# Kernel optimization log

Measured on AMD Instinct MI355X. Metric: run time of the kernel, lower is better.

## Reference

```python
import jax, jax.numpy as jnp
import numpy as np
import math

H = 16          # attn_heads
DK = 64         # features_dec // attn_heads
NEG = -1e9      # additive causal mask value
EPS = 1e-6      # LayerNorm eps (annotated transformer)


def get_slopes(n):
    def p2(m):
        start = 2.0 ** (-(2.0 ** (-(math.log2(m) - 3))))
        return [start * start ** i for i in range(m)]
    if math.log2(n).is_integer():
        return p2(n)
    cp = 2 ** math.floor(math.log2(n))
    return p2(cp) + get_slopes(2 * cp)[0::2][: n - cp]


def setup_inputs() -> dict:
    key = jax.random.key(0)
    ks = jax.random.split(key, 12)
    B, S, FT, FDZ, FDEC, FD = 8, 1024, 16, 768, 1024, 16

    def lin(k, out_d, in_d):
        return jax.random.normal(k, (out_d, in_d), jnp.float32) / np.float32(np.sqrt(in_d))

    return {
        "z_sample": jax.random.normal(ks[0], (B, FDZ), jnp.float32),
        "r_traj": jax.random.normal(ks[1], (B, S, FT), jnp.float32),
        "dense_w": lin(ks[2], FDEC, FDZ + FT), "dense_b": jnp.zeros((FDEC,), jnp.float32),
        "ln_g": jnp.ones((FDEC,), jnp.float32), "ln_b": jnp.zeros((FDEC,), jnp.float32),
        "wq": lin(ks[3], FDEC, FDEC), "bq": jnp.zeros((FDEC,), jnp.float32),
        "wk": lin(ks[4], FDEC, FDEC), "bk": jnp.zeros((FDEC,), jnp.float32),
        "wv": lin(ks[5], FDEC, FDEC), "bv": jnp.zeros((FDEC,), jnp.float32),
        "wo": lin(ks[6], FDEC, FDEC), "bo": jnp.zeros((FDEC,), jnp.float32),
        "dec_w": lin(ks[7], FD, FDEC), "dec_b": jnp.zeros((FD,), jnp.float32),
    }


def reference(z_sample, r_traj, dense_w, dense_b, ln_g, ln_b,
              wq, bq, wk, bk, wv, bv, wo, bo, dec_w, dec_b):
    B, S, _ = r_traj.shape
    # concat trajectory features with broadcast latent sample -> [B,S,in_size]
    x = jnp.concatenate(
        [r_traj, jnp.broadcast_to(z_sample[:, None, :], (B, S, z_sample.shape[-1]))], axis=-1)
    x = x @ dense_w.T + dense_b  # [B,S,FDEC]

    # causal additive mask + ALiBi bias: bias[h,i,j] = causal(i,j) + slope_h * j
    slopes = jnp.asarray(get_slopes(H), jnp.float32)
    causal = jnp.triu(jnp.full((S, S), NEG, jnp.float32), k=1)
    bias = causal[None, :, :] + slopes[:, None, None] * jnp.arange(S, dtype=jnp.float32)[None, None, :]  # [H,S,S]

    # pre-norm sublayer: x + attn(LN(x))  (dropout=0 / eval)
    mu = x.mean(-1, keepdims=True)
    var = x.var(-1, keepdims=True)
    xn = ln_g * (x - mu) / jnp.sqrt(var + EPS) + ln_b

    def heads(w, b):
        return (xn @ w.T + b).reshape(B, S, H, DK).transpose(0, 2, 1, 3)  # [B,H,S,DK]

    q, k, v = heads(wq, bq), heads(wk, bk), heads(wv, bv)
    scores = jnp.einsum('bhid,bhjd->bhij', q, k) / np.float32(np.sqrt(DK)) + bias[None]
    attn = jax.nn.softmax(scores, axis=-1)
    o = jnp.einsum('bhij,bhjd->bhid', attn, v).transpose(0, 2, 1, 3).reshape(B, S, H * DK)
    x = x + o @ wo.T + bo

    # decode_state then transpose(-2,-1) -> [B, features_d, S]
    return (x @ dec_w.T + dec_b).transpose(0, 2, 1)
```

## Files before the change

kernel.cpp:

```cpp
#include <hip/hip_runtime.h>

static constexpr int Bn   = 8;
static constexpr int S    = 1024;
static constexpr int FT   = 16;
static constexpr int FDZ  = 768;
static constexpr int INK  = 784;
static constexpr int FDEC = 1024;
static constexpr int M    = Bn * S;
static constexpr int H    = 16;
static constexpr int FD   = 16;

typedef __bf16 bf16x8 __attribute__((ext_vector_type(8)));
typedef float  f32x4  __attribute__((ext_vector_type(4)));

__device__ __forceinline__ unsigned short f2b(float f) {
  return __builtin_bit_cast(unsigned short, static_cast<__bf16>(f));
}
__device__ __forceinline__ float b2f(unsigned short u) {
  return (float)__builtin_bit_cast(__bf16, u);
}

__device__ __forceinline__ void gload16(const void* g, void* l) {
  __builtin_amdgcn_global_load_lds(
      (const __attribute__((address_space(1))) unsigned int*)g,
      (__attribute__((address_space(3))) unsigned int*)l, 16, 0, 0);
}

__global__ __launch_bounds__(256) void k_prep(const float* __restrict__ dnw,
                                              const float* __restrict__ wq,
                                              const float* __restrict__ wk,
                                              const float* __restrict__ wv,
                                              const float* __restrict__ wo,
                                              const float* __restrict__ dcw,
                                              const float* __restrict__ bq,
                                              const float* __restrict__ bk,
                                              const float* __restrict__ bv,
                                              unsigned short* __restrict__ w3,
                                              unsigned short* __restrict__ wob,
                                              unsigned short* __restrict__ dwb,
                                              float* __restrict__ b3,
                                              unsigned short* __restrict__ wt16) {
  const int bid = blockIdx.x, tid = threadIdx.x;
  const int c = tid * 4;
  if (bid < 3072) {
    const int r = bid;
    const float* src = (r < 1024) ? wq : (r < 2048 ? wk : wv);
    const int rr = r & 1023;
    float4 v = *reinterpret_cast<const float4*>(&src[(size_t)rr * 1024 + c]);
    unsigned short o4[4] = {f2b(v.x), f2b(v.y), f2b(v.z), f2b(v.w)};
    *reinterpret_cast<uint2*>(&w3[(size_t)r * 1024 + c]) = *reinterpret_cast<uint2*>(o4);
  } else if (bid < 4096) {
    const int r = bid - 3072;
    float4 v = *reinterpret_cast<const float4*>(&wo[(size_t)r * 1024 + c]);
    unsigned short o4[4] = {f2b(v.x), f2b(v.y), f2b(v.z), f2b(v.w)};
    *reinterpret_cast<uint2*>(&wob[(size_t)r * 1024 + c]) = *reinterpret_cast<uint2*>(o4);
  } else if (bid < 4112) {
    const int r = bid - 4096;
    float4 v = *reinterpret_cast<const float4*>(&dcw[(size_t)r * 1024 + c]);
    unsigned short o4[4] = {f2b(v.x), f2b(v.y), f2b(v.z), f2b(v.w)};
    *reinterpret_cast<uint2*>(&dwb[(size_t)r * 1024 + c]) = *reinterpret_cast<uint2*>(o4);
  } else if (bid < 4115) {
    const int r = bid - 4112;
    const float* s = (r == 0) ? bq : (r == 1 ? bk : bv);
    *reinterpret_cast<float4*>(&b3[r * 1024 + c]) =
        *reinterpret_cast<const float4*>(&s[c]);
  } else {
    const int idx = (bid - 4115) * 256 + tid;
    const int k = idx >> 10, cc = idx & 1023;
    wt16[k * 1024 + cc] = f2b(dnw[(size_t)cc * INK + k]);
  }
}

__global__ __launch_bounds__(256) void k_za(const float* __restrict__ z,
                                            const float* __restrict__ dnw,
                                            float* __restrict__ za) {
  const int tid = threadIdx.x, lane = tid & 63, w = tid >> 6;
  const int idx = blockIdx.x * 4 + w;
  const int col = idx >> 3, b = idx & 7;
  const float* wp = &dnw[(size_t)col * INK + FT];
  const float* zp = &z[b * FDZ];
  float s = 0.f;
#pragma unroll
  for (int i = 0; i < 12; i++) {
    int k = lane + i * 64;
    s += wp[k] * zp[k];
  }
  for (int off = 32; off; off >>= 1) s += __shfl_down(s, off);
  if (lane == 0) za[b * 1024 + col] = s;
}

__global__ __launch_bounds__(256) void k_dense_ln(const float* __restrict__ rt,
                                                  const float* __restrict__ za,
                                                  const float* __restrict__ dnb,
                                                  const float* __restrict__ lng,
                                                  const float* __restrict__ lnb,
                                                  const unsigned short* __restrict__ wt16g,
                                                  unsigned short* __restrict__ xres,
                                                  unsigned short* __restrict__ xn) {
  __shared__ unsigned short wt[16 * 1024];
  __shared__ float ss[4], qq[4];
  const int tid = threadIdx.x, lane = tid & 63, wv = tid >> 6;
  const int c0 = tid * 4;
#pragma unroll
  for (int i = 0; i < 8; i++)
    reinterpret_cast<uint4*>(wt)[tid + 256 * i] =
        reinterpret_cast<const uint4*>(wt16g)[tid + 256 * i];
  const float4 bv  = *reinterpret_cast<const float4*>(&dnb[c0]);
  const float4 gv  = *reinterpret_cast<const float4*>(&lng[c0]);
  const float4 bev = *reinterpret_cast<const float4*>(&lnb[c0]);
  __syncthreads();

  for (int r = 0; r < 4; ++r) {
    const int m = blockIdx.x * 4 + r;
    const int b = m >> 10;
    float rtv[16];
    {
      float4 t0 = *reinterpret_cast<const float4*>(&rt[m * 16 + 0]);
      float4 t1 = *reinterpret_cast<const float4*>(&rt[m * 16 + 4]);
      float4 t2 = *reinterpret_cast<const float4*>(&rt[m * 16 + 8]);
      float4 t3 = *reinterpret_cast<const float4*>(&rt[m * 16 + 12]);
      rtv[0]=t0.x; rtv[1]=t0.y; rtv[2]=t0.z; rtv[3]=t0.w;
      rtv[4]=t1.x; rtv[5]=t1.y; rtv[6]=t1.z; rtv[7]=t1.w;
      rtv[8]=t2.x; rtv[9]=t2.y; rtv[10]=t2.z; rtv[11]=t2.w;
      rtv[12]=t3.x; rtv[13]=t3.y; rtv[14]=t3.z; rtv[15]=t3.w;
    }
    float4 zav = *reinterpret_cast<const float4*>(&za[b * 1024 + c0]);
    float acc[4] = {zav.x + bv.x, zav.y + bv.y, zav.z + bv.z, zav.w + bv.w};
#pragma unroll
    for (int k = 0; k < 16; ++k) {
      uint2 wraw = *reinterpret_cast<const uint2*>(&wt[k * 1024 + c0]);
      const unsigned short* wp = reinterpret_cast<const unsigned short*>(&wraw);
      float rk = rtv[k];
      acc[0] += rk * b2f(wp[0]);
      acc[1] += rk * b2f(wp[1]);
      acc[2] += rk * b2f(wp[2]);
      acc[3] += rk * b2f(wp[3]);
    }
    float s = acc[0] + acc[1] + acc[2] + acc[3];
    float q = acc[0]*acc[0] + acc[1]*acc[1] + acc[2]*acc[2] + acc[3]*acc[3];
    for (int off = 32; off; off >>= 1) { s += __shfl_down(s, off); q += __shfl_down(q, off); }
    if (lane == 0) { ss[wv] = s; qq[wv] = q; }
    __syncthreads();
    float St = ss[0] + ss[1] + ss[2] + ss[3];
    float Qt = qq[0] + qq[1] + qq[2] + qq[3];
    float mu  = St * (1.f / 1024.f);
    float var = Qt * (1.f / 1024.f) - mu * mu;
    float rstd = rsqrtf(var + 1e-6f);
    unsigned short xo[4], no[4];
    xo[0] = f2b(acc[0]); no[0] = f2b(gv.x * (acc[0] - mu) * rstd + bev.x);
    xo[1] = f2b(acc[1]); no[1] = f2b(gv.y * (acc[1] - mu) * rstd + bev.y);
    xo[2] = f2b(acc[2]); no[2] = f2b(gv.z * (acc[2] - mu) * rstd + bev.z);
    xo[3] = f2b(acc[3]); no[3] = f2b(gv.w * (acc[3] - mu) * rstd + bev.w);
    *reinterpret_cast<uint2*>(&xres[(size_t)m * 1024 + c0]) = *reinterpret_cast<uint2*>(xo);
    *reinterpret_cast<uint2*>(&xn[(size_t)m * 1024 + c0])   = *reinterpret_cast<uint2*>(no);
    __syncthreads();
  }
}

template<int EPI>
__global__ __launch_bounds__(512, 4) void k_gemm2(const unsigned short* __restrict__ A, int lda,
                                                  const unsigned short* __restrict__ Bw, int ldb,
                                                  int K, int N,
                                                  const float* __restrict__ bias,
                                                  float* __restrict__ Cf,
                                                  unsigned short* __restrict__ Cb) {
  __shared__ __align__(16) unsigned short As[3 * 256 * 32];
  __shared__ __align__(16) unsigned short Bs[3 * 128 * 32];
  const int tid = threadIdx.x, lane = tid & 63, w = tid >> 6;
  const int wr = w >> 1, wc = w & 1;
  const int lr = lane & 15, lg = lane >> 4;

  const int xcd = blockIdx.x & 7;
  const int j   = blockIdx.x >> 3;
  const int m0  = (xcd * 4 + (j & 3)) * 256;
  const int n0  = (j >> 2) * 128;

  const int nt = K >> 5;

  const int giA0 = w * 64 + lane;
  const int rA0 = giA0 >> 2, cA0 = (giA0 & 3) ^ ((rA0 >> 1) & 3);
  const int giA1 = 512 + w * 64 + lane;
  const int rA1 = giA1 >> 2, cA1 = (giA1 & 3) ^ ((rA1 >> 1) & 3);
  const int giB0 = w * 64 + lane;
  const int rB0 = giB0 >> 2, cB0 = (giB0 & 3) ^ ((rB0 >> 1) & 3);
  const unsigned short* srcA0 = A + (size_t)(m0 + rA0) * lda + cA0 * 8;
  const unsigned short* srcA1 = A + (size_t)(m0 + rA1) * lda + cA1 * 8;
  const unsigned short* srcB0 = Bw + (size_t)(n0 + rB0) * ldb + cB0 * 8;
  const int dA0 = (w * 64) * 8;
  const int dA1 = (512 + w * 64) * 8;
  const int dB0 = (w * 64) * 8;

  int offA[4], offB[4];
#pragma unroll
  for (int mi = 0; mi < 4; mi++) {
    int r = wr * 64 + mi * 16 + lr;
    offA[mi] = r * 32 + (lg ^ ((r >> 1) & 3)) * 8;
  }
#pragma unroll
  for (int ni = 0; ni < 4; ni++) {
    int r = wc * 64 + ni * 16 + lr;
    offB[ni] = r * 32 + (lg ^ ((r >> 1) & 3)) * 8;
  }

  f32x4 acc[4][4];
#pragma unroll
  for (int i = 0; i < 4; i++)
#pragma unroll
    for (int j2 = 0; j2 < 4; j2++)
#pragma unroll
      for (int e = 0; e < 4; e++) acc[i][j2][e] = 0.f;

  auto stage = [&](int tt) {
    const int sl = tt % 3;
    const size_t ko = (size_t)tt * 32;
    gload16(srcA0 + ko, &As[sl * 8192 + dA0]);
    gload16(srcA1 + ko, &As[sl * 8192 + dA1]);
    gload16(srcB0 + ko, &Bs[sl * 4096 + dB0]);
  };
  auto compute = [&](int tt) {
    const int sa = (tt % 3) * 8192;
    const int sb = (tt % 3) * 4096;
    bf16x8 af[4], bfr[4];
#pragma unroll
    for (int mi = 0; mi < 4; mi++)
      af[mi] = *reinterpret_cast<const bf16x8*>(&As[sa + offA[mi]]);
#pragma unroll
    for (int ni = 0; ni < 4; ni++)
      bfr[ni] = *reinterpret_cast<const bf16x8*>(&Bs[sb + offB[ni]]);
    __builtin_amdgcn_s_setprio(1);
#pragma unroll
    for (int mi = 0; mi < 4; mi++)
#pragma unroll
      for (int ni = 0; ni < 4; ni++)
        acc[mi][ni] = __builtin_amdgcn_mfma_f32_16x16x32_bf16(af[mi], bfr[ni], acc[mi][ni], 0, 0, 0);
    __builtin_amdgcn_s_setprio(0);
  };

  stage(0); stage(1);

  int t = 0;
  for (; t < nt - 2; ++t) {
    asm volatile("s_waitcnt vmcnt(3)" ::: "memory");
    __builtin_amdgcn_s_barrier();
    stage(t + 2);
    compute(t);
  }
  asm volatile("s_waitcnt vmcnt(3)" ::: "memory");
  __builtin_amdgcn_s_barrier();
  compute(t); ++t;
  asm volatile("s_waitcnt vmcnt(0)" ::: "memory");
  __builtin_amdgcn_s_barrier();
  compute(t);

#pragma unroll
  for (int mi = 0; mi < 4; mi++)
#pragma unroll
    for (int ni = 0; ni < 4; ni++) {
      int col = n0 + wc * 64 + ni * 16 + lr;
      float bv = bias ? bias[col] : 0.f;
#pragma unroll
      for (int jj = 0; jj < 4; jj++) {
        int row = m0 + wr * 64 + mi * 16 + lg * 4 + jj;
        float v = acc[mi][ni][jj] + bv;
        if constexpr (EPI == 0) {
          Cf[(size_t)row * N + col] = v;
        } else {
          Cb[(size_t)row * N + col] = f2b(v);
        }
      }
    }
}

template<int EPI>
__global__ __launch_bounds__(256, 3) void k_gemm1(const unsigned short* __restrict__ A, int lda,
                                                  const unsigned short* __restrict__ Bw, int ldb,
                                                  int K, int N,
                                                  const float* __restrict__ bias,
                                                  const unsigned short* __restrict__ res,
                                                  unsigned short* __restrict__ Cb) {
  __shared__ __align__(16) unsigned short As[3 * 128 * 32];
  __shared__ __align__(16) unsigned short Bs[3 * 128 * 32];
  const int tid = threadIdx.x, lane = tid & 63, w = tid >> 6;
  const int wr = w >> 1, wc = w & 1;
  const int lr = lane & 15, lg = lane >> 4;

  const int xcd = blockIdx.x & 7;
  const int j   = blockIdx.x >> 3;
  const int m0  = (xcd * 8 + (j & 7)) * 128;
  const int n0  = (j >> 3) * 128;

  const int nt = K >> 5;

  const int g0 = tid;
  const int r0g = g0 >> 2, c0g = (g0 & 3) ^ ((r0g >> 1) & 3);
  const int g1 = tid + 256;
  const int r1g = g1 >> 2, c1g = (g1 & 3) ^ ((r1g >> 1) & 3);
  const unsigned short* srcA0 = A + (size_t)(m0 + r0g) * lda + c0g * 8;
  const unsigned short* srcA1 = A + (size_t)(m0 + r1g) * lda + c1g * 8;
  const unsigned short* srcB0 = Bw + (size_t)(n0 + r0g) * ldb + c0g * 8;
  const unsigned short* srcB1 = Bw + (size_t)(n0 + r1g) * ldb + c1g * 8;
  const int d0 = (w * 64) * 8;
  const int d1 = (256 + w * 64) * 8;

  int offA[4], offB[4];
#pragma unroll
  for (int mi = 0; mi < 4; mi++) {
    int r = wr * 64 + mi * 16 + lr;
    offA[mi] = r * 32 + (lg ^ ((r >> 1) & 3)) * 8;
  }
#pragma unroll
  for (int ni = 0; ni < 4; ni++) {
    int r = wc * 64 + ni * 16 + lr;
    offB[ni] = r * 32 + (lg ^ ((r >> 1) & 3)) * 8;
  }

  f32x4 acc[4][4];
#pragma unroll
  for (int i = 0; i < 4; i++)
#pragma unroll
    for (int j2 = 0; j2 < 4; j2++)
#pragma unroll
      for (int e = 0; e < 4; e++) acc[i][j2][e] = 0.f;

  auto stage = [&](int tt) {
    const int sl = tt % 3;
    const size_t ko = (size_t)tt * 32;
    gload16(srcA0 + ko, &As[sl * 4096 + d0]);
    gload16(srcA1 + ko, &As[sl * 4096 + d1]);
    gload16(srcB0 + ko, &Bs[sl * 4096 + d0]);
    gload16(srcB1 + ko, &Bs[sl * 4096 + d1]);
  };
  auto compute = [&](int tt) {
    const int sl = (tt % 3) * 4096;
    bf16x8 af[4], bfr[4];
#pragma unroll
    for (int mi = 0; mi < 4; mi++)
      af[mi] = *reinterpret_cast<const bf16x8*>(&As[sl + offA[mi]]);
#pragma unroll
    for (int ni = 0; ni < 4; ni++)
      bfr[ni] = *reinterpret_cast<const bf16x8*>(&Bs[sl + offB[ni]]);
    __builtin_amdgcn_s_setprio(1);
#pragma unroll
    for (int mi = 0; mi < 4; mi++)
#pragma unroll
      for (int ni = 0; ni < 4; ni++)
        acc[mi][ni] = __builtin_amdgcn_mfma_f32_16x16x32_bf16(af[mi], bfr[ni], acc[mi][ni], 0, 0, 0);
    __builtin_amdgcn_s_setprio(0);
  };

  stage(0); stage(1);

  int t = 0;
  for (; t < nt - 2; ++t) {
    asm volatile("s_waitcnt vmcnt(4)" ::: "memory");
    __builtin_amdgcn_s_barrier();
    stage(t + 2);
    compute(t);
  }
  asm volatile("s_waitcnt vmcnt(4)" ::: "memory");
  __builtin_amdgcn_s_barrier();
  compute(t); ++t;
  asm volatile("s_waitcnt vmcnt(0)" ::: "memory");
  __builtin_amdgcn_s_barrier();
  compute(t);

#pragma unroll
  for (int mi = 0; mi < 4; mi++)
#pragma unroll
    for (int ni = 0; ni < 4; ni++) {
      int col = n0 + wc * 64 + ni * 16 + lr;
      float bv = bias ? bias[col] : 0.f;
#pragma unroll
      for (int jj = 0; jj < 4; jj++) {
        int row = m0 + wr * 64 + mi * 16 + lg * 4 + jj;
        float v = acc[mi][ni][jj] + bv;
        size_t o = (size_t)row * N + col;
        if constexpr (EPI == 2) {
          Cb[o] = f2b(b2f(res[o]) + v);
        } else {
          Cb[o] = f2b(v);
        }
      }
    }
}

__global__ __launch_bounds__(512, 4) void k_attn(const unsigned short* __restrict__ qkv,
                                                 unsigned short* __restrict__ o) {
  __shared__ unsigned short Ks[2][64][72];
  __shared__ unsigned short Vt[2][64][72];
  __shared__ unsigned short Pl[8][16][72];
  const int tid = threadIdx.x, lane = tid & 63, w = tid >> 6;
  const int bh = blockIdx.x, b = bh >> 4, h = bh & 15;
  const int lr = lane & 15, lg = lane >> 4, lg4 = lg * 4;
  const int krow = tid >> 3, c8 = (tid & 7) << 3;
  const int kb8 = krow >> 3, kl = krow & 7, vq = tid & 7;
  const float slope2 = exp2f(-0.5f * (float)(h + 1)) * 1.44269504f;
  const float sc2 = 0.125f * 1.44269504f;

  for (int ph = 0; ph < 2; ++ph) {
    const int qb = ph ? (7 - (int)blockIdx.y) : (int)blockIdx.y;
    const int q0 = qb * 128;
    const int qlo = q0 + w * 16;
    const int qa = qlo + lr;

    bf16x8 qf0, qf1;
    {
      const unsigned short* qp = &qkv[(size_t)(b * 1024 + qlo + lr) * 3072 + h * 64];
      qf0 = *reinterpret_cast<const bf16x8*>(qp + lg * 8);
      qf1 = *reinterpret_cast<const bf16x8*>(qp + 32 + lg * 8);
    }
    float mrun = -3.0e38f, lrun = 0.f;
    f32x4 accO[4];
    for (int dn = 0; dn < 4; dn++)
      for (int e = 0; e < 4; e++) accO[dn][e] = 0.f;

    const int nt = 2 * qb + 2;
    uint4 kr, vr;
    {
      const size_t base = (size_t)(b * 1024 + krow) * 3072 + h * 64;
      kr = *reinterpret_cast<const uint4*>(&qkv[base + 1024 + c8]);
      vr = *reinterpret_cast<const uint4*>(&qkv[base + 2048 + c8]);
    }
    *reinterpret_cast<uint4*>(&Ks[0][krow][c8]) = kr;
    {
      const unsigned short* vs = reinterpret_cast<const unsigned short*>(&vr);
      for (int jj = 0; jj < 8; jj++)
        Vt[0][c8 + jj][((kb8 ^ vq) << 3) | kl] = vs[jj];
    }
    __syncthreads();

    for (int kt = 0; kt < nt; ++kt) {
      const int kb = kt << 6;
      const int cb = kt & 1, nb = cb ^ 1;
      const bool hn = (kt + 1 < nt);
      if (hn) {
        const size_t base = (size_t)(b * 1024 + kb + 64 + krow) * 3072 + h * 64;
        kr = *reinterpret_cast<const uint4*>(&qkv[base + 1024 + c8]);
        vr = *reinterpret_cast<const uint4*>(&qkv[base + 2048 + c8]);
      }
      const bool act = (kb <= qlo + 15);
      float f = 1.f;
      if (act) {
        f32x4 sf[4];
        for (int kn = 0; kn < 4; kn++) {
          f32x4 zz;
          for (int e = 0; e < 4; e++) zz[e] = 0.f;
          bf16x8 kf0 = *reinterpret_cast<const bf16x8*>(&Ks[cb][kn * 16 + lr][lg * 8]);
          bf16x8 kf1 = *reinterpret_cast<const bf16x8*>(&Ks[cb][kn * 16 + lr][32 + lg * 8]);
          zz = __builtin_amdgcn_mfma_f32_16x16x32_bf16(kf0, qf0, zz, 0, 0, 0);
          zz = __builtin_amdgcn_mfma_f32_16x16x32_bf16(kf1, qf1, zz, 0, 0, 0);
          sf[kn] = zz;
        }
        const bool needmask = (kb + 63 > qlo);
        float sc[4][4];
        float ml = -3.0e38f;
        for (int kn = 0; kn < 4; kn++) {
          float alib = slope2 * (float)(kb + kn * 16 + lg4);
          for (int jj = 0; jj < 4; jj++) {
            float v = fmaf(sf[kn][jj], sc2, alib + slope2 * (float)jj);
            if (needmask && (kb + kn * 16 + lg4 + jj > qa)) v = -3.0e38f;
            sc[kn][jj] = v;
            ml = fmaxf(ml, v);
          }
        }
        ml = fmaxf(ml, __shfl_xor(ml, 16));
        ml = fmaxf(ml, __shfl_xor(ml, 32));
        float mnew = fmaxf(mrun, ml);
        f = exp2f(mrun - mnew);
        float rs = 0.f;
        for (int kn = 0; kn < 4; kn++) {
          __bf16 pb[4];
          for (int jj = 0; jj < 4; jj++) {
            float pv = exp2f(sc[kn][jj] - mnew);
            rs += pv;
            pb[jj] = (__bf16)pv;
          }
          *reinterpret_cast<uint2*>(&Pl[w][lr][kn * 16 + lg4]) =
              *reinterpret_cast<uint2*>(pb);
        }
        rs += __shfl_xor(rs, 16);
        rs += __shfl_xor(rs, 32);
        lrun = lrun * f + rs;
        mrun = mnew;
      }
      if (hn) {
        *reinterpret_cast<uint4*>(&Ks[nb][krow][c8]) = kr;
        const unsigned short* vs = reinterpret_cast<const unsigned short*>(&vr);
        for (int jj = 0; jj < 8; jj++)
          Vt[nb][c8 + jj][((kb8 ^ vq) << 3) | kl] = vs[jj];
      }
      if (act) {
        float fj[4];
        for (int jj = 0; jj < 4; jj++) fj[jj] = __shfl(f, (lane & 48) | (lg4 + jj));
        for (int dn = 0; dn < 4; dn++)
          for (int jj = 0; jj < 4; jj++) accO[dn][jj] *= fj[jj];
        asm volatile("s_waitcnt lgkmcnt(0)" ::: "memory");
        for (int ks = 0; ks < 2; ks++) {
          bf16x8 pa = *reinterpret_cast<const bf16x8*>(&Pl[w][lr][ks * 32 + lg * 8]);
          for (int dn = 0; dn < 4; dn++) {
            int d = dn * 16 + lr;
            bf16x8 vb = *reinterpret_cast<const bf16x8*>(
                &Vt[cb][d][(((ks * 4 + lg) ^ (d >> 3)) << 3)]);
            accO[dn] = __builtin_amdgcn_mfma_f32_16x16x32_bf16(pa, vb, accO[dn], 0, 0, 0);
          }
        }
      }
      __syncthreads();
    }
    float linv[4];
    for (int jj = 0; jj < 4; jj++)
      linv[jj] = 1.f / __shfl(lrun, (lane & 48) | (lg4 + jj));
    for (int dn = 0; dn < 4; dn++)
      for (int jj = 0; jj < 4; jj++) {
        int row = qlo + lg4 + jj;
        int d = dn * 16 + lr;
        o[(size_t)(b * 1024 + row) * 1024 + h * 64 + d] = f2b(accO[dn][jj] * linv[jj]);
      }
  }
}

__global__ __launch_bounds__(256) void k_dec(const unsigned short* __restrict__ xb,
                                             const unsigned short* __restrict__ dw,
                                             const float* __restrict__ db,
                                             float* __restrict__ out) {
  const int tid = threadIdx.x, lane = tid & 63, w = tid >> 6;
  const int lr = lane & 15, lg = lane >> 4;
  const int sb = blockIdx.x * 4 + w;
  const int r0 = sb * 16;
  f32x4 acc;
  for (int e = 0; e < 4; e++) acc[e] = 0.f;
  const unsigned short* arow = &xb[(size_t)(r0 + lr) * 1024];
  const unsigned short* brow = &dw[(size_t)lr * 1024];
  for (int k0 = 0; k0 < 1024; k0 += 32) {
    bf16x8 af = *reinterpret_cast<const bf16x8*>(arow + k0 + lg * 8);
    bf16x8 bf = *reinterpret_cast<const bf16x8*>(brow + k0 + lg * 8);
    acc = __builtin_amdgcn_mfma_f32_16x16x32_bf16(af, bf, acc, 0, 0, 0);
  }
  const int b = r0 >> 10;
  const int sl = (r0 & 1023) + lg * 4;
  float bias = db[lr];
  float4 res;
  res.x = acc[0] + bias; res.y = acc[1] + bias; res.z = acc[2] + bias; res.w = acc[3] + bias;
  *reinterpret_cast<float4*>(&out[(size_t)(b * 16 + lr) * 1024 + sl]) = res;
}

extern "C" void kernel_launch(void* const* d_in, const int* in_sizes, int n_in,
                              void* d_out, int out_size, void* d_ws, size_t ws_size,
                              hipStream_t stream) {
  (void)in_sizes; (void)n_in; (void)out_size;
  const float* z   = (const float*)d_in[0];
  const float* rt  = (const float*)d_in[1];
  const float* dnw = (const float*)d_in[2];
  const float* dnb = (const float*)d_in[3];
  const float* lng = (const float*)d_in[4];
  const float* lnb = (const float*)d_in[5];
  const float* wq  = (const float*)d_in[6];
  const float* bq  = (const float*)d_in[7];
  const float* wk  = (const float*)d_in[8];
  const float* bk  = (const float*)d_in[9];
  const float* wv  = (const float*)d_in[10];
  const float* bv  = (const float*)d_in[11];
  const float* wo  = (const float*)d_in[12];
  const float* bo  = (const float*)d_in[13];
  const float* dcw = (const float*)d_in[14];
  const float* dcb = (const float*)d_in[15];
  float* out = (float*)d_out;

  char* p = (char*)d_ws;
  unsigned short* xres = (unsigned short*)p; p += (size_t)M * FDEC * 2;
  unsigned short* xn   = (unsigned short*)p; p += (size_t)M * FDEC * 2;
  unsigned short* w3   = (unsigned short*)p; p += (size_t)3 * FDEC * FDEC * 2;
  float* b3            = (float*)p;          p += (size_t)3 * FDEC * 4;
  unsigned short* qkv  = (unsigned short*)p; p += (size_t)M * 3 * FDEC * 2;
  unsigned short* ob   = (unsigned short*)p; p += (size_t)M * FDEC * 2;
  unsigned short* wob  = (unsigned short*)p; p += (size_t)FDEC * FDEC * 2;
  unsigned short* dwb  = (unsigned short*)p; p += (size_t)FD * FDEC * 2;
  float* za            = (float*)p;          p += (size_t)8 * 1024 * 4;
  unsigned short* wt16 = (unsigned short*)p; p += (size_t)16 * 1024 * 2;
  if ((size_t)(p - (char*)d_ws) > ws_size) return;

  k_prep<<<4179, 256, 0, stream>>>(dnw, wq, wk, wv, wo, dcw, bq, bk, bv,
                                   w3, wob, dwb, b3, wt16);
  k_za<<<2048, 256, 0, stream>>>(z, dnw, za);
  k_dense_ln<<<2048, 256, 0, stream>>>(rt, za, dnb, lng, lnb, wt16, xres, xn);
  k_gemm2<1><<<(M / 256) * (3 * FDEC / 128), 512, 0, stream>>>(xn, FDEC, w3, FDEC, FDEC, 3 * FDEC, b3, nullptr, qkv);
  k_attn<<<dim3(Bn * H, 4), 512, 0, stream>>>(qkv, ob);
  k_gemm1<2><<<(M / 128) * (FDEC / 128), 256, 0, stream>>>(ob, FDEC, wob, FDEC, FDEC, FDEC, bo, xres, xn);
  k_dec<<<M / 64, 256, 0, stream>>>(xn, dwb, dcb, out);
}
```

Baseline: 185.5 us.

## Fold output projection into decoder via precombined weight, drop O-projection GEMM

Because the decoder is linear, dec_w·(x + o·Woᵀ + bo) is rewritten as dec_w·x + (dec_w·Wo)·o + (dec_w·bo + dec_b). A new kernel builds the 16x1024 combined weight and bias, so the full 8192x1024x1024 output-projection GEMM goes away and the decoder kernel does two thin K=1024 MFMA passes instead. The QKV projection also switches from the 256x128-tile gemm2 kernel to the 128x128-tile gemm1 kernel. In exchange, the combined weight is rounded to bf16 and a strided weight reduction runs on every call.

```diff
diff --git a/kernel.cpp b/kernel.cpp
--- a/kernel.cpp
+++ b/kernel.cpp
@@ -30,13 +30,11 @@
                                               const float* __restrict__ wq,
                                               const float* __restrict__ wk,
                                               const float* __restrict__ wv,
-                                              const float* __restrict__ wo,
                                               const float* __restrict__ dcw,
                                               const float* __restrict__ bq,
                                               const float* __restrict__ bk,
                                               const float* __restrict__ bv,
                                               unsigned short* __restrict__ w3,
-                                              unsigned short* __restrict__ wob,
                                               unsigned short* __restrict__ dwb,
                                               float* __restrict__ b3,
                                               unsigned short* __restrict__ wt16) {
@@ -49,25 +47,55 @@
     float4 v = *reinterpret_cast<const float4*>(&src[(size_t)rr * 1024 + c]);
     unsigned short o4[4] = {f2b(v.x), f2b(v.y), f2b(v.z), f2b(v.w)};
     *reinterpret_cast<uint2*>(&w3[(size_t)r * 1024 + c]) = *reinterpret_cast<uint2*>(o4);
-  } else if (bid < 4096) {
+  } else if (bid < 3088) {
     const int r = bid - 3072;
-    float4 v = *reinterpret_cast<const float4*>(&wo[(size_t)r * 1024 + c]);
-    unsigned short o4[4] = {f2b(v.x), f2b(v.y), f2b(v.z), f2b(v.w)};
-    *reinterpret_cast<uint2*>(&wob[(size_t)r * 1024 + c]) = *reinterpret_cast<uint2*>(o4);
-  } else if (bid < 4112) {
-    const int r = bid - 4096;
     float4 v = *reinterpret_cast<const float4*>(&dcw[(size_t)r * 1024 + c]);
     unsigned short o4[4] = {f2b(v.x), f2b(v.y), f2b(v.z), f2b(v.w)};
     *reinterpret_cast<uint2*>(&dwb[(size_t)r * 1024 + c]) = *reinterpret_cast<uint2*>(o4);
-  } else if (bid < 4115) {
-    const int r = bid - 4112;
+  } else if (bid < 3091) {
+    const int r = bid - 3088;
     const float* s = (r == 0) ? bq : (r == 1 ? bk : bv);
     *reinterpret_cast<float4*>(&b3[r * 1024 + c]) =
         *reinterpret_cast<const float4*>(&s[c]);
   } else {
-    const int idx = (bid - 4115) * 256 + tid;
+    const int idx = (bid - 3091) * 256 + tid;
     const int k = idx >> 10, cc = idx & 1023;
     wt16[k * 1024 + cc] = f2b(dnw[(size_t)cc * INK + k]);
+  }
+}
+
+__global__ __launch_bounds__(256) void k_wcomb(const float* __restrict__ dcw,
+                                               const float* __restrict__ wo,
+                                               const float* __restrict__ bo,
+                                               const float* __restrict__ dcb,
+                                               unsigned short* __restrict__ wcombb,
+                                               float* __restrict__ bias2) {
+  const int tid = threadIdx.x, lane = tid & 63, w = tid >> 6;
+  if (blockIdx.x < 4096) {
+    const int idx = blockIdx.x * 4 + w;
+    const int i = idx >> 10, jcol = idx & 1023;
+    const float* dp = &dcw[(size_t)i * 1024];
+    float s = 0.f;
+#pragma unroll
+    for (int t = 0; t < 16; t++) {
+      int k = lane + t * 64;
+      s += dp[k] * wo[(size_t)k * 1024 + jcol];
+    }
+    for (int off = 32; off; off >>= 1) s += __shfl_down(s, off);
+    if (lane == 0) wcombb[i * 1024 + jcol] = f2b(s);
+  } else {
+    for (int q = 0; q < 4; q++) {
+      int f = w * 4 + q;
+      const float* dp = &dcw[(size_t)f * 1024];
+      float s = 0.f;
+#pragma unroll
+      for (int t = 0; t < 16; t++) {
+        int k = lane + t * 64;
+        s += dp[k] * bo[k];
+      }
+      for (int off = 32; off; off >>= 1) s += __shfl_down(s, off);
+      if (lane == 0) bias2[f] = s + dcb[f];
+    }
   }
 }
 
@@ -158,125 +186,10 @@
 }
 
 template<int EPI>
-__global__ __launch_bounds__(512, 4) void k_gemm2(const unsigned short* __restrict__ A, int lda,
-                                                  const unsigned short* __restrict__ Bw, int ldb,
-                                                  int K, int N,
-                                                  const float* __restrict__ bias,
-                                                  float* __restrict__ Cf,
-                                                  unsigned short* __restrict__ Cb) {
-  __shared__ __align__(16) unsigned short As[3 * 256 * 32];
-  __shared__ __align__(16) unsigned short Bs[3 * 128 * 32];
-  const int tid = threadIdx.x, lane = tid & 63, w = tid >> 6;
-  const int wr = w >> 1, wc = w & 1;
-  const int lr = lane & 15, lg = lane >> 4;
-
-  const int xcd = blockIdx.x & 7;
-  const int j   = blockIdx.x >> 3;
-  const int m0  = (xcd * 4 + (j & 3)) * 256;
-  const int n0  = (j >> 2) * 128;
-
-  const int nt = K >> 5;
-
-  const int giA0 = w * 64 + lane;
-  const int rA0 = giA0 >> 2, cA0 = (giA0 & 3) ^ ((rA0 >> 1) & 3);
-  const int giA1 = 512 + w * 64 + lane;
-  const int rA1 = giA1 >> 2, cA1 = (giA1 & 3) ^ ((rA1 >> 1) & 3);
-  const int giB0 = w * 64 + lane;
-  const int rB0 = giB0 >> 2, cB0 = (giB0 & 3) ^ ((rB0 >> 1) & 3);
-  const unsigned short* srcA0 = A + (size_t)(m0 + rA0) * lda + cA0 * 8;
-  const unsigned short* srcA1 = A + (size_t)(m0 + rA1) * lda + cA1 * 8;
-  const unsigned short* srcB0 = Bw + (size_t)(n0 + rB0) * ldb + cB0 * 8;
-  const int dA0 = (w * 64) * 8;
-  const int dA1 = (512 + w * 64) * 8;
-  const int dB0 = (w * 64) * 8;
-
-  int offA[4], offB[4];
-#pragma unroll
-  for (int mi = 0; mi < 4; mi++) {
-    int r = wr * 64 + mi * 16 + lr;
-    offA[mi] = r * 32 + (lg ^ ((r >> 1) & 3)) * 8;
-  }
-#pragma unroll
-  for (int ni = 0; ni < 4; ni++) {
-    int r = wc * 64 + ni * 16 + lr;
-    offB[ni] = r * 32 + (lg ^ ((r >> 1) & 3)) * 8;
-  }
-
-  f32x4 acc[4][4];
-#pragma unroll
-  for (int i = 0; i < 4; i++)
-#pragma unroll
-    for (int j2 = 0; j2 < 4; j2++)
-#pragma unroll
-      for (int e = 0; e < 4; e++) acc[i][j2][e] = 0.f;
-
-  auto stage = [&](int tt) {
-    const int sl = tt % 3;
-    const size_t ko = (size_t)tt * 32;
-    gload16(srcA0 + ko, &As[sl * 8192 + dA0]);
-    gload16(srcA1 + ko, &As[sl * 8192 + dA1]);
-    gload16(srcB0 + ko, &Bs[sl * 4096 + dB0]);
-  };
-  auto compute = [&](int tt) {
-    const int sa = (tt % 3) * 8192;
-    const int sb = (tt % 3) * 4096;
-    bf16x8 af[4], bfr[4];
-#pragma unroll
-    for (int mi = 0; mi < 4; mi++)
-      af[mi] = *reinterpret_cast<const bf16x8*>(&As[sa + offA[mi]]);
-#pragma unroll
-    for (int ni = 0; ni < 4; ni++)
-      bfr[ni] = *reinterpret_cast<const bf16x8*>(&Bs[sb + offB[ni]]);
-    __builtin_amdgcn_s_setprio(1);
-#pragma unroll
-    for (int mi = 0; mi < 4; mi++)
-#pragma unroll
-      for (int ni = 0; ni < 4; ni++)
-        acc[mi][ni] = __builtin_amdgcn_mfma_f32_16x16x32_bf16(af[mi], bfr[ni], acc[mi][ni], 0, 0, 0);
-    __builtin_amdgcn_s_setprio(0);
-  };
-
-  stage(0); stage(1);
-
-  int t = 0;
-  for (; t < nt - 2; ++t) {
-    asm volatile("s_waitcnt vmcnt(3)" ::: "memory");
-    __builtin_amdgcn_s_barrier();
-    stage(t + 2);
-    compute(t);
-  }
-  asm volatile("s_waitcnt vmcnt(3)" ::: "memory");
-  __builtin_amdgcn_s_barrier();
-  compute(t); ++t;
-  asm volatile("s_waitcnt vmcnt(0)" ::: "memory");
-  __builtin_amdgcn_s_barrier();
-  compute(t);
-
-#pragma unroll
-  for (int mi = 0; mi < 4; mi++)
-#pragma unroll
-    for (int ni = 0; ni < 4; ni++) {
-      int col = n0 + wc * 64 + ni * 16 + lr;
-      float bv = bias ? bias[col] : 0.f;
-#pragma unroll
-      for (int jj = 0; jj < 4; jj++) {
-        int row = m0 + wr * 64 + mi * 16 + lg * 4 + jj;
-        float v = acc[mi][ni][jj] + bv;
-        if constexpr (EPI == 0) {
-          Cf[(size_t)row * N + col] = v;
-        } else {
-          Cb[(size_t)row * N + col] = f2b(v);
-        }
-      }
-    }
-}
-
-template<int EPI>
 __global__ __launch_bounds__(256, 3) void k_gemm1(const unsigned short* __restrict__ A, int lda,
                                                   const unsigned short* __restrict__ Bw, int ldb,
                                                   int K, int N,
                                                   const float* __restrict__ bias,
-                                                  const unsigned short* __restrict__ res,
                                                   unsigned short* __restrict__ Cb) {
   __shared__ __align__(16) unsigned short As[3 * 128 * 32];
   __shared__ __align__(16) unsigned short Bs[3 * 128 * 32];
@@ -374,12 +287,7 @@
       for (int jj = 0; jj < 4; jj++) {
         int row = m0 + wr * 64 + mi * 16 + lg * 4 + jj;
         float v = acc[mi][ni][jj] + bv;
-        size_t o = (size_t)row * N + col;
-        if constexpr (EPI == 2) {
-          Cb[o] = f2b(b2f(res[o]) + v);
-        } else {
-          Cb[o] = f2b(v);
-        }
+        Cb[(size_t)row * N + col] = f2b(v);
       }
     }
 }
@@ -519,26 +427,33 @@
   }
 }
 
-__global__ __launch_bounds__(256) void k_dec(const unsigned short* __restrict__ xb,
-                                             const unsigned short* __restrict__ dw,
-                                             const float* __restrict__ db,
-                                             float* __restrict__ out) {
+__global__ __launch_bounds__(256) void k_dec2(const unsigned short* __restrict__ xres,
+                                              const unsigned short* __restrict__ ob,
+                                              const unsigned short* __restrict__ dwb,
+                                              const unsigned short* __restrict__ wcombb,
+                                              const float* __restrict__ bias2,
+                                              float* __restrict__ out) {
   const int tid = threadIdx.x, lane = tid & 63, w = tid >> 6;
   const int lr = lane & 15, lg = lane >> 4;
   const int sb = blockIdx.x * 4 + w;
   const int r0 = sb * 16;
   f32x4 acc;
   for (int e = 0; e < 4; e++) acc[e] = 0.f;
-  const unsigned short* arow = &xb[(size_t)(r0 + lr) * 1024];
-  const unsigned short* brow = &dw[(size_t)lr * 1024];
+  const unsigned short* arow1 = &xres[(size_t)(r0 + lr) * 1024];
+  const unsigned short* arow2 = &ob[(size_t)(r0 + lr) * 1024];
+  const unsigned short* brow1 = &dwb[(size_t)lr * 1024];
+  const unsigned short* brow2 = &wcombb[(size_t)lr * 1024];
   for (int k0 = 0; k0 < 1024; k0 += 32) {
-    bf16x8 af = *reinterpret_cast<const bf16x8*>(arow + k0 + lg * 8);
-    bf16x8 bf = *reinterpret_cast<const bf16x8*>(brow + k0 + lg * 8);
-    acc = __builtin_amdgcn_mfma_f32_16x16x32_bf16(af, bf, acc, 0, 0, 0);
+    bf16x8 a1 = *reinterpret_cast<const bf16x8*>(arow1 + k0 + lg * 8);
+    bf16x8 b1 = *reinterpret_cast<const bf16x8*>(brow1 + k0 + lg * 8);
+    acc = __builtin_amdgcn_mfma_f32_16x16x32_bf16(a1, b1, acc, 0, 0, 0);
+    bf16x8 a2 = *reinterpret_cast<const bf16x8*>(arow2 + k0 + lg * 8);
+    bf16x8 b2 = *reinterpret_cast<const bf16x8*>(brow2 + k0 + lg * 8);
+    acc = __builtin_amdgcn_mfma_f32_16x16x32_bf16(a2, b2, acc, 0, 0, 0);
   }
   const int b = r0 >> 10;
   const int sl = (r0 & 1023) + lg * 4;
-  float bias = db[lr];
+  float bias = bias2[lr];
   float4 res;
   res.x = acc[0] + bias; res.y = acc[1] + bias; res.z = acc[2] + bias; res.w = acc[3] + bias;
   *reinterpret_cast<float4*>(&out[(size_t)(b * 16 + lr) * 1024 + sl]) = res;
@@ -567,24 +482,25 @@
   float* out = (float*)d_out;
 
   char* p = (char*)d_ws;
-  unsigned short* xres = (unsigned short*)p; p += (size_t)M * FDEC * 2;
-  unsigned short* xn   = (unsigned short*)p; p += (size_t)M * FDEC * 2;
-  unsigned short* w3   = (unsigned short*)p; p += (size_t)3 * FDEC * FDEC * 2;
-  float* b3            = (float*)p;          p += (size_t)3 * FDEC * 4;
-  unsigned short* qkv  = (unsigned short*)p; p += (size_t)M * 3 * FDEC * 2;
-  unsigned short* ob   = (unsigned short*)p; p += (size_t)M * FDEC * 2;
-  unsigned short* wob  = (unsigned short*)p; p += (size_t)FDEC * FDEC * 2;
-  unsigned short* dwb  = (unsigned short*)p; p += (size_t)FD * FDEC * 2;
-  float* za            = (float*)p;          p += (size_t)8 * 1024 * 4;
-  unsigned short* wt16 = (unsigned short*)p; p += (size_t)16 * 1024 * 2;
+  unsigned short* xres  = (unsigned short*)p; p += (size_t)M * FDEC * 2;
+  unsigned short* xn    = (unsigned short*)p; p += (size_t)M * FDEC * 2;
+  unsigned short* w3    = (unsigned short*)p; p += (size_t)3 * FDEC * FDEC * 2;
+  float* b3             = (float*)p;          p += (size_t)3 * FDEC * 4;
+  unsigned short* qkv   = (unsigned short*)p; p += (size_t)M * 3 * FDEC * 2;
+  unsigned short* ob    = (unsigned short*)p; p += (size_t)M * FDEC * 2;
+  unsigned short* dwb   = (unsigned short*)p; p += (size_t)FD * FDEC * 2;
+  unsigned short* wcombb= (unsigned short*)p; p += (size_t)FD * FDEC * 2;
+  float* bias2          = (float*)p;          p += (size_t)FD * 4;
+  float* za             = (float*)p;          p += (size_t)8 * 1024 * 4;
+  unsigned short* wt16  = (unsigned short*)p; p += (size_t)16 * 1024 * 2;
   if ((size_t)(p - (char*)d_ws) > ws_size) return;
 
-  k_prep<<<4179, 256, 0, stream>>>(dnw, wq, wk, wv, wo, dcw, bq, bk, bv,
-                                   w3, wob, dwb, b3, wt16);
+  k_prep<<<3155, 256, 0, stream>>>(dnw, wq, wk, wv, dcw, bq, bk, bv,
+                                   w3, dwb, b3, wt16);
+  k_wcomb<<<4097, 256, 0, stream>>>(dcw, wo, bo, dcb, wcombb, bias2);
   k_za<<<2048, 256, 0, stream>>>(z, dnw, za);
   k_dense_ln<<<2048, 256, 0, stream>>>(rt, za, dnb, lng, lnb, wt16, xres, xn);
-  k_gemm2<1><<<(M / 256) * (3 * FDEC / 128), 512, 0, stream>>>(xn, FDEC, w3, FDEC, FDEC, 3 * FDEC, b3, nullptr, qkv);
+  k_gemm1<1><<<(M / 128) * (3 * FDEC / 128), 256, 0, stream>>>(xn, FDEC, w3, FDEC, FDEC, 3 * FDEC, b3, qkv);
   k_attn<<<dim3(Bn * H, 4), 512, 0, stream>>>(qkv, ob);
-  k_gemm1<2><<<(M / 128) * (FDEC / 128), 256, 0, stream>>>(ob, FDEC, wob, FDEC, FDEC, FDEC, bo, xres, xn);
-  k_dec<<<M / 64, 256, 0, stream>>>(xn, dwb, dcb, out);
-}
+  k_dec2<<<M / 64, 256, 0, stream>>>(xres, ob, dwb, wcombb, bias2, out);
+}
```

Result: slower. 226.2 us (+22.0%).
